# Optimization experiments

Measured on AMD Instinct MI355X. Metric: run time of the kernel, lower is better.

## Reference

```python
import jax, jax.numpy as jnp
import numpy as np

DIM = 64
HID = DIM // 8  # 8, hidden width of pos_fc / attn_fc
B, N, V = 1024, 64, 8
NUM_IDS = 10


def setup_inputs() -> dict:
    key = jax.random.key(0)
    ks = jax.random.split(key, 24)
    stdv = 1.0 / np.sqrt(DIM * DIM)
    inp = {
        "q": jax.random.normal(ks[0], (B, N, DIM), jnp.float32),
        "k": jax.random.normal(ks[1], (B, N, V, DIM), jnp.float32),
        "pos": jax.random.normal(ks[2], (B, N, V, 4), jnp.float32),
        "strength": jax.random.normal(ks[3], (512,), jnp.float32),
        # learned params
        "q_tbl": jax.random.uniform(ks[4], (NUM_IDS, DIM * DIM), jnp.float32, -stdv, stdv),
        "k_tbl": jax.random.uniform(ks[5], (NUM_IDS, DIM * DIM), jnp.float32, -stdv, stdv),
        "v_tbl": jax.random.uniform(ks[6], (NUM_IDS, DIM * DIM), jnp.float32, -stdv, stdv),
        "pos_w1": jax.random.normal(ks[7], (4, HID), jnp.float32) * 0.5,
        "pos_b1": jax.random.normal(ks[8], (HID,), jnp.float32) * 0.1,
        "pos_w2": jax.random.normal(ks[9], (HID, DIM), jnp.float32) * 0.2,
        "pos_b2": jax.random.normal(ks[10], (DIM,), jnp.float32) * 0.1,
        "attn_w1": jax.random.normal(ks[11], (DIM, HID), jnp.float32) * 0.1,
        "attn_b1": jax.random.normal(ks[12], (HID,), jnp.float32) * 0.1,
        "attn_w2": jax.random.normal(ks[13], (HID, DIM), jnp.float32) * 0.2,
        "attn_b2": jax.random.normal(ks[14], (DIM,), jnp.float32) * 0.1,
        "out_w": jax.random.normal(ks[15], (DIM, DIM), jnp.float32) * 0.1,
        "out_b": jax.random.normal(ks[16], (DIM,), jnp.float32) * 0.1,
        "str_w": jax.random.normal(ks[17], (512, DIM), jnp.float32) * 0.04,
        "str_b": jax.random.normal(ks[18], (DIM,), jnp.float32) * 0.1,
        # int args
        "mask": jax.random.randint(ks[19], (B, N, V, 1), 0, 2, jnp.int32),
        "embed_id1": 3,
    }
    return inp


def reference(q, k, pos, strength, q_tbl, k_tbl, v_tbl,
              pos_w1, pos_b1, pos_w2, pos_b2,
              attn_w1, attn_b1, attn_w2, attn_b2,
              out_w, out_b, str_w, str_b, mask, embed_id1):
    s = strength @ str_w + str_b                       # [DIM]
    Wq = q_tbl[embed_id1].reshape(DIM, DIM)
    Wk = k_tbl[embed_id1].reshape(DIM, DIM)
    Wv = v_tbl[embed_id1].reshape(DIM, DIM)
    # F.linear(x, W) = x @ W.T ; note v is computed from k (as in source)
    qh = q @ Wq.T + s                                  # [B,N,DIM]
    kh = k @ Wk.T + s                                  # [B,N,V,DIM]
    vh = k @ Wv.T + s                                  # [B,N,V,DIM]
    p = jax.nn.relu(pos @ pos_w1 + pos_b1) @ pos_w2 + pos_b2   # [B,N,V,DIM]
    attn = kh - qh[:, :, None, :] + p                  # [B,N,V,DIM]
    attn = jax.nn.relu(attn @ attn_w1 + attn_b1) @ attn_w2 + attn_b2
    attn = jnp.where(mask == 0, jnp.float32(-1e9), attn)
    attn = jax.nn.softmax(attn, axis=-2)               # softmax over views V
    x = ((vh + p) * attn).sum(axis=2)                  # [B,N,DIM]
    x = x @ out_w + out_b
    return x
```

## Files before the change

kernel.cpp:

```cpp
#include <hip/hip_runtime.h>

#define TBL 4096

#define WS_S    0
#define WS_AT   64
#define WS_BQT  (64 + 512)
#define WS_CT   (64 + 1024)
#define WS_C0   (64 + 1024 + 64)

typedef __attribute__((ext_vector_type(8))) short bf16x8;
typedef __attribute__((ext_vector_type(4))) float f32x4;

__device__ inline short f2bf(float f) {
    union { float f; unsigned u; } v; v.f = f;
    unsigned r = v.u + 0x7fffu + ((v.u >> 16) & 1u);
    return (short)(r >> 16);
}

__device__ inline bf16x8 pack8(const float* x) {
    bf16x8 r;
    #pragma unroll
    for (int i = 0; i < 8; ++i) r[i] = f2bf(x[i]);
    return r;
}

__device__ inline bf16x8 loadpack(const float* p) {
    float4 a = *(const float4*)p;
    float4 b = *(const float4*)(p + 4);
    float t[8] = {a.x, a.y, a.z, a.w, b.x, b.y, b.z, b.w};
    return pack8(t);
}

__device__ inline bf16x8 loadpackneg(const float* p) {
    float4 a = *(const float4*)p;
    float4 b = *(const float4*)(p + 4);
    float t[8] = {-a.x, -a.y, -a.z, -a.w, -b.x, -b.y, -b.z, -b.w};
    return pack8(t);
}

__global__ __launch_bounds__(256) void precompute_kernel(
    const float* __restrict__ strength, const float* __restrict__ str_w,
    const float* __restrict__ str_b,
    const float* __restrict__ q_tbl, const float* __restrict__ k_tbl,
    const float* __restrict__ attn_w1, const float* __restrict__ attn_b1,
    const float* __restrict__ pos_w2, const float* __restrict__ pos_b2,
    const int* __restrict__ embed_id, float* __restrict__ ws)
{
    __shared__ float red[4][64];
    const int t = threadIdx.x;
    const int blk = blockIdx.x;
    const int id = embed_id[0];
    if (blk == 0) {
        const int d = t & 63, part = t >> 6;
        float acc = 0.f;
        for (int i = part * 128; i < part * 128 + 128; ++i)
            acc += strength[i] * str_w[i * 64 + d];
        red[part][d] = acc;
        __syncthreads();
        if (t < 64)
            ws[WS_S + t] = red[0][t] + red[1][t] + red[2][t] + red[3][t] + str_b[t];
    } else if (blk <= 2) {
        const int h = (blk - 1) * 4 + (t >> 6);
        const int j = t & 63;
        const float* W = k_tbl + (size_t)id * TBL;
        float acc = 0.f;
        for (int d = 0; d < 64; ++d) acc += W[d * 64 + j] * attn_w1[d * 8 + h];
        ws[WS_AT + h * 64 + j] = acc;
    } else if (blk <= 4) {
        const int h = (blk - 3) * 4 + (t >> 6);
        const int j = t & 63;
        const float* W = q_tbl + (size_t)id * TBL;
        float acc = 0.f;
        for (int d = 0; d < 64; ++d) acc += W[d * 64 + j] * attn_w1[d * 8 + h];
        ws[WS_BQT + h * 64 + j] = acc;
    } else {
        if (t < 64) {
            const int h = t >> 3, g = t & 7;
            float acc = 0.f;
            for (int d = 0; d < 64; ++d) acc += pos_w2[g * 64 + d] * attn_w1[d * 8 + h];
            ws[WS_CT + t] = acc;
        } else if (t < 72) {
            const int h = t - 64;
            float acc = attn_b1[h];
            for (int d = 0; d < 64; ++d) acc += pos_b2[d] * attn_w1[d * 8 + h];
            ws[WS_C0 + h] = acc;
        }
    }
}

__global__ __launch_bounds__(256, 3) void attn2d_main(
    const float* __restrict__ q, const float* __restrict__ k,
    const float* __restrict__ pos, const float* __restrict__ v_tbl,
    const float* __restrict__ pos_w1, const float* __restrict__ pos_b1,
    const float* __restrict__ pos_w2, const float* __restrict__ pos_b2,
    const float* __restrict__ attn_w2, const float* __restrict__ attn_b2,
    const float* __restrict__ out_w, const float* __restrict__ out_b,
    const int* __restrict__ mask, const int* __restrict__ embed_id,
    const float* __restrict__ ws, float* __restrict__ out)
{
    __shared__ float rhid_lds[4][16 * 12];
    __shared__ float x_lds[4][8 * 68];

    const int tid  = threadIdx.x;
    const int lane = tid & 63;
    const int wiv  = __builtin_amdgcn_readfirstlane(tid >> 6);
    const int q4   = lane >> 4;
    const int col  = lane & 15;

    float* rh_w = rhid_lds[wiv];
    float* x_w  = x_lds[wiv];

    const int wid = blockIdx.x * 4 + wiv;
    const int id  = embed_id[0];

    bf16x8 Bv[4][2];
    #pragma unroll
    for (int t = 0; t < 4; ++t)
        #pragma unroll
        for (int c = 0; c < 2; ++c)
            Bv[t][c] = loadpack(v_tbl + (size_t)id * TBL +
                                (t * 16 + col) * 64 + c * 32 + q4 * 8);
    bf16x8 Bh[4];
    {
        bf16x8 z{};
        #pragma unroll
        for (int c = 0; c < 2; ++c)
            Bh[c] = (col < 8) ? loadpack(ws + WS_AT + col * 64 + c * 32 + q4 * 8) : z;
        #pragma unroll
        for (int c = 0; c < 2; ++c)
            Bh[2 + c] = (col < 8) ? loadpackneg(ws + WS_BQT + col * 64 + c * 32 + q4 * 8) : z;
    }
    bf16x8 Bct{};
    if (q4 == 0 && col < 8) Bct = loadpack(ws + WS_CT + col * 8);
    bf16x8 Bw2[4], Bpw2[4];
    {
        bf16x8 z{};
        #pragma unroll
        for (int t = 0; t < 4; ++t) {
            if (q4 == 0) {
                float t0[8], t1[8];
                #pragma unroll
                for (int j = 0; j < 8; ++j) {
                    t0[j] = attn_w2[j * 64 + t * 16 + col];
                    t1[j] = pos_w2[j * 64 + t * 16 + col];
                }
                Bw2[t] = pack8(t0); Bpw2[t] = pack8(t1);
            } else { Bw2[t] = z; Bpw2[t] = z; }
        }
    }

    float b2a4[4], sb4[4], ob4[4];
    #pragma unroll
    for (int t = 0; t < 4; ++t) {
        b2a4[t] = attn_b2[t * 16 + col];
        sb4[t]  = ws[WS_S + t * 16 + col] + pos_b2[t * 16 + col];
        ob4[t]  = out_b[t * 16 + col];
    }
    const float c0r = (col < 8) ? ws[WS_C0 + col] : 0.f;

    for (int it = 0; it < 4; ++it) {
        const int pair = wid * 4 + it;
        const int bn0  = pair * 2;

        bf16x8 Ak[2], Aq[2];
        #pragma unroll
        for (int c = 0; c < 2; ++c)
            Ak[c] = loadpack(k + ((size_t)pair * 16 + col) * 64 + c * 32 + q4 * 8);
        #pragma unroll
        for (int c = 0; c < 2; ++c)
            Aq[c] = loadpack(q + (size_t)(bn0 + (col >> 3)) * 64 + c * 32 + q4 * 8);

        const int4 mk = *(const int4*)(mask + (size_t)pair * 16 + q4 * 4);

        bf16x8 Ahp{};
        if (lane < 16) {
            float4 pp = *(const float4*)(pos + ((size_t)pair * 16 + lane) * 4);
            float hv[8];
            #pragma unroll
            for (int g = 0; g < 8; ++g)
                hv[g] = fmaxf(pos_b1[g] + pp.x * pos_w1[g] + pp.y * pos_w1[8 + g] +
                              pp.z * pos_w1[16 + g] + pp.w * pos_w1[24 + g], 0.f);
            Ahp = pack8(hv);
        }

        f32x4 acch = {0.f, 0.f, 0.f, 0.f};
        acch = __builtin_amdgcn_mfma_f32_16x16x32_bf16(Ak[0], Bh[0], acch, 0, 0, 0);
        acch = __builtin_amdgcn_mfma_f32_16x16x32_bf16(Ak[1], Bh[1], acch, 0, 0, 0);
        acch = __builtin_amdgcn_mfma_f32_16x16x32_bf16(Aq[0], Bh[2], acch, 0, 0, 0);
        acch = __builtin_amdgcn_mfma_f32_16x16x32_bf16(Aq[1], Bh[3], acch, 0, 0, 0);
        acch = __builtin_amdgcn_mfma_f32_16x16x32_bf16(Ahp,   Bct,   acch, 0, 0, 0);
        if (col < 8) {
            #pragma unroll
            for (int r = 0; r < 4; ++r)
                rh_w[(q4 * 4 + r) * 12 + col] = fmaxf(acch[r] + c0r, 0.f);
        }

        bf16x8 Arh{};
        if (lane < 16) Arh = loadpack(&rh_w[lane * 12]);

        #pragma unroll
        for (int t = 0; t < 4; ++t) {
            f32x4 av = {0.f, 0.f, 0.f, 0.f};
            av = __builtin_amdgcn_mfma_f32_16x16x32_bf16(Ak[0], Bv[t][0], av, 0, 0, 0);
            av = __builtin_amdgcn_mfma_f32_16x16x32_bf16(Ak[1], Bv[t][1], av, 0, 0, 0);
            av = __builtin_amdgcn_mfma_f32_16x16x32_bf16(Ahp,   Bpw2[t],  av, 0, 0, 0);
            f32x4 al = {0.f, 0.f, 0.f, 0.f};
            al = __builtin_amdgcn_mfma_f32_16x16x32_bf16(Arh, Bw2[t], al, 0, 0, 0);

            float att[4];
            att[0] = mk.x ? (al[0] + b2a4[t]) : -1e9f;
            att[1] = mk.y ? (al[1] + b2a4[t]) : -1e9f;
            att[2] = mk.z ? (al[2] + b2a4[t]) : -1e9f;
            att[3] = mk.w ? (al[3] + b2a4[t]) : -1e9f;

            float mp = fmaxf(fmaxf(att[0], att[1]), fmaxf(att[2], att[3]));
            float mm = fmaxf(mp, __shfl_xor(mp, 16));
            float e0 = __expf(att[0] - mm), e1 = __expf(att[1] - mm);
            float e2 = __expf(att[2] - mm), e3 = __expf(att[3] - mm);
            float sp = e0 + e1 + e2 + e3;
            float ss = sp + __shfl_xor(sp, 16);
            float xp = e0 * (av[0] + sb4[t]) + e1 * (av[1] + sb4[t])
                     + e2 * (av[2] + sb4[t]) + e3 * (av[3] + sb4[t]);
            float x = (xp + __shfl_xor(xp, 16)) * __builtin_amdgcn_rcpf(ss);
            if ((q4 & 1) == 0)
                x_w[(it * 2 + (q4 >> 1)) * 68 + t * 16 + col] = x;
        }
    }

    bf16x8 Ax[2]{};
    if (col < 8) {
        #pragma unroll
        for (int c = 0; c < 2; ++c)
            Ax[c] = loadpack(&x_w[col * 68 + c * 32 + q4 * 8]);
    }
    #pragma unroll
    for (int t = 0; t < 4; ++t) {
        bf16x8 Bo0, Bo1;
        {
            float t0[8], t1[8];
            #pragma unroll
            for (int jj = 0; jj < 8; ++jj) {
                t0[jj] = out_w[(q4 * 8 + jj) * 64 + t * 16 + col];
                t1[jj] = out_w[(32 + q4 * 8 + jj) * 64 + t * 16 + col];
            }
            Bo0 = pack8(t0); Bo1 = pack8(t1);
        }
        f32x4 a = {0.f, 0.f, 0.f, 0.f};
        a = __builtin_amdgcn_mfma_f32_16x16x32_bf16(Ax[0], Bo0, a, 0, 0, 0);
        a = __builtin_amdgcn_mfma_f32_16x16x32_bf16(Ax[1], Bo1, a, 0, 0, 0);
        #pragma unroll
        for (int r = 0; r < 4; ++r) {
            const int row = q4 * 4 + r;
            if (row < 8)
                out[((size_t)wid * 8 + row) * 64 + t * 16 + col] = a[r] + ob4[t];
        }
    }
}

extern "C" void kernel_launch(void* const* d_in, const int* in_sizes, int n_in,
                              void* d_out, int out_size, void* d_ws, size_t ws_size,
                              hipStream_t stream) {
    const float* q        = (const float*)d_in[0];
    const float* k        = (const float*)d_in[1];
    const float* pos      = (const float*)d_in[2];
    const float* strength = (const float*)d_in[3];
    const float* q_tbl    = (const float*)d_in[4];
    const float* k_tbl    = (const float*)d_in[5];
    const float* v_tbl    = (const float*)d_in[6];
    const float* pos_w1   = (const float*)d_in[7];
    const float* pos_b1   = (const float*)d_in[8];
    const float* pos_w2   = (const float*)d_in[9];
    const float* pos_b2   = (const float*)d_in[10];
    const float* attn_w1  = (const float*)d_in[11];
    const float* attn_b1  = (const float*)d_in[12];
    const float* attn_w2  = (const float*)d_in[13];
    const float* attn_b2  = (const float*)d_in[14];
    const float* out_w    = (const float*)d_in[15];
    const float* out_b    = (const float*)d_in[16];
    const float* str_w    = (const float*)d_in[17];
    const float* str_b    = (const float*)d_in[18];
    const int*   mask     = (const int*)d_in[19];
    const int*   embed    = (const int*)d_in[20];
    float* ws  = (float*)d_ws;
    float* out = (float*)d_out;

    hipLaunchKernelGGL(precompute_kernel, dim3(6), dim3(256), 0, stream,
                       strength, str_w, str_b, q_tbl, k_tbl, attn_w1, attn_b1,
                       pos_w2, pos_b2, embed, ws);
    hipLaunchKernelGGL(attn2d_main, dim3(2048), dim3(256), 0, stream,
                       q, k, pos, v_tbl, pos_w1, pos_b1, pos_w2, pos_b2,
                       attn_w2, attn_b2, out_w, out_b, mask, embed, ws, out);
}
```

Before: 291.0 us.

## Prepack bf16 weights, double-buffer k loads, process 8 pairs per wave

Adds a pack kernel that converts the weight matrices (v table, out_w, attn/pos weights) to bf16 in MFMA-ready layout once, so each wave loads them directly instead of gathering and converting floats. The main kernel now handles 16 rows per wave over 8 iterations with a grid of half the size, and prefetches the next iteration's k, pos and mask into registers. The q projection is computed once per wave, the pos MLP first layer moves onto MFMA, and k is truncated to bf16 via byte permutes instead of rounding. It costs an extra kernel launch and more registers, and the truncation slightly changes numerics.

Result: no change. 292.9 us (+0.6%).

```diff
diff --git a/kernel.cpp b/kernel.cpp
--- a/kernel.cpp
+++ b/kernel.cpp
@@ -4,9 +4,19 @@
 
 #define WS_S    0
 #define WS_AT   64
-#define WS_BQT  (64 + 512)
-#define WS_CT   (64 + 1024)
-#define WS_C0   (64 + 1024 + 64)
+#define WS_BQT  576
+#define WS_CT   1088
+#define WS_C0   1152
+#define WS_F32_END 1536
+#define PB_AT   0
+#define PB_BQN  512
+#define PB_CT   1024
+#define PB_W2T  1088
+#define PB_PW2T 1600
+#define PB_PW1  2112
+#define PB_VT   2176
+#define PB_OWT  6272
+#define PB_END  10368
 
 typedef __attribute__((ext_vector_type(8))) short bf16x8;
 typedef __attribute__((ext_vector_type(4))) float f32x4;
@@ -31,11 +41,13 @@
     return pack8(t);
 }
 
-__device__ inline bf16x8 loadpackneg(const float* p) {
-    float4 a = *(const float4*)p;
-    float4 b = *(const float4*)(p + 4);
-    float t[8] = {-a.x, -a.y, -a.z, -a.w, -b.x, -b.y, -b.z, -b.w};
-    return pack8(t);
+__device__ inline bf16x8 pack8t(float4 a, float4 b) {
+    union { unsigned u[4]; bf16x8 v; } r;
+    r.u[0] = __builtin_amdgcn_perm(__float_as_uint(a.y), __float_as_uint(a.x), 0x07060302u);
+    r.u[1] = __builtin_amdgcn_perm(__float_as_uint(a.w), __float_as_uint(a.z), 0x07060302u);
+    r.u[2] = __builtin_amdgcn_perm(__float_as_uint(b.y), __float_as_uint(b.x), 0x07060302u);
+    r.u[3] = __builtin_amdgcn_perm(__float_as_uint(b.w), __float_as_uint(b.z), 0x07060302u);
+    return r.v;
 }
 
 __global__ __launch_bounds__(256) void precompute_kernel(
@@ -88,18 +100,51 @@
     }
 }
 
+__global__ __launch_bounds__(256) void pack_kernel(
+    const float* __restrict__ v_tbl,
+    const float* __restrict__ pos_w1, const float* __restrict__ pos_w2,
+    const float* __restrict__ attn_w2, const float* __restrict__ out_w,
+    const int* __restrict__ embed_id, float* __restrict__ ws)
+{
+    short* pk = (short*)(ws + WS_F32_END);
+    const int i = blockIdx.x * 256 + threadIdx.x;
+    if (i >= PB_END) return;
+    const int id = embed_id[0];
+    if (i < 512) {
+        pk[i] = f2bf(ws[WS_AT + i]);
+    } else if (i < 1024) {
+        pk[i] = f2bf(-ws[WS_BQT + (i - 512)]);
+    } else if (i < 1088) {
+        pk[i] = f2bf(ws[WS_CT + (i - 1024)]);
+    } else if (i < 1600) {
+        const int idx = i - 1088, d = idx >> 3, h = idx & 7;
+        pk[i] = f2bf(attn_w2[h * 64 + d]);
+    } else if (i < 2112) {
+        const int idx = i - 1600, d = idx >> 3, h = idx & 7;
+        pk[i] = f2bf(pos_w2[h * 64 + d]);
+    } else if (i < 2176) {
+        const int idx = i - 2112, h = idx >> 3, j = idx & 7;
+        pk[i] = (j < 4) ? f2bf(pos_w1[j * 8 + h]) : (short)0;
+    } else if (i < 6272) {
+        pk[i] = f2bf(v_tbl[(size_t)id * TBL + (i - 2176)]);
+    } else {
+        const int idx = i - 6272, e = idx >> 6, d = idx & 63;
+        pk[i] = f2bf(out_w[d * 64 + e]);
+    }
+}
+
 __global__ __launch_bounds__(256, 3) void attn2d_main(
     const float* __restrict__ q, const float* __restrict__ k,
-    const float* __restrict__ pos, const float* __restrict__ v_tbl,
-    const float* __restrict__ pos_w1, const float* __restrict__ pos_b1,
-    const float* __restrict__ pos_w2, const float* __restrict__ pos_b2,
-    const float* __restrict__ attn_w2, const float* __restrict__ attn_b2,
-    const float* __restrict__ out_w, const float* __restrict__ out_b,
-    const int* __restrict__ mask, const int* __restrict__ embed_id,
+    const float* __restrict__ pos,
+    const float* __restrict__ pos_b1, const float* __restrict__ pos_b2,
+    const float* __restrict__ attn_b2, const float* __restrict__ out_b,
+    const int* __restrict__ mask,
     const float* __restrict__ ws, float* __restrict__ out)
 {
-    __shared__ float rhid_lds[4][16 * 12];
-    __shared__ float x_lds[4][8 * 68];
+    __shared__ __align__(16) short hp_bf[4][16 * 8];
+    __shared__ __align__(16) short rh_bf[4][16 * 8];
+    __shared__ __align__(16) float qB_lds[4][16 * 8];
+    __shared__ __align__(16) short x_bf[4][16 * 72];
 
     const int tid  = threadIdx.x;
     const int lane = tid & 63;
@@ -107,46 +152,32 @@
     const int q4   = lane >> 4;
     const int col  = lane & 15;
 
-    float* rh_w = rhid_lds[wiv];
-    float* x_w  = x_lds[wiv];
+    short* hp_w = hp_bf[wiv];
+    short* rh_w = rh_bf[wiv];
+    float* qB_w = qB_lds[wiv];
+    short* x_w  = x_bf[wiv];
 
     const int wid = blockIdx.x * 4 + wiv;
-    const int id  = embed_id[0];
+    const short* pk = (const short*)(ws + WS_F32_END);
+    const bf16x8 z{};
 
     bf16x8 Bv[4][2];
     #pragma unroll
     for (int t = 0; t < 4; ++t)
         #pragma unroll
         for (int c = 0; c < 2; ++c)
-            Bv[t][c] = loadpack(v_tbl + (size_t)id * TBL +
-                                (t * 16 + col) * 64 + c * 32 + q4 * 8);
-    bf16x8 Bh[4];
-    {
-        bf16x8 z{};
-        #pragma unroll
-        for (int c = 0; c < 2; ++c)
-            Bh[c] = (col < 8) ? loadpack(ws + WS_AT + col * 64 + c * 32 + q4 * 8) : z;
-        #pragma unroll
-        for (int c = 0; c < 2; ++c)
-            Bh[2 + c] = (col < 8) ? loadpackneg(ws + WS_BQT + col * 64 + c * 32 + q4 * 8) : z;
-    }
-    bf16x8 Bct{};
-    if (q4 == 0 && col < 8) Bct = loadpack(ws + WS_CT + col * 8);
+            Bv[t][c] = *(const bf16x8*)&pk[PB_VT + (t * 16 + col) * 64 + c * 32 + q4 * 8];
+    bf16x8 Bh[2];
+    #pragma unroll
+    for (int c = 0; c < 2; ++c)
+        Bh[c] = (col < 8) ? *(const bf16x8*)&pk[PB_AT + col * 64 + c * 32 + q4 * 8] : z;
+    const bf16x8 Bct  = (q4 == 0 && col < 8) ? *(const bf16x8*)&pk[PB_CT + col * 8] : z;
+    const bf16x8 Bpw1 = (q4 == 0 && col < 8) ? *(const bf16x8*)&pk[PB_PW1 + col * 8] : z;
     bf16x8 Bw2[4], Bpw2[4];
-    {
-        bf16x8 z{};
-        #pragma unroll
-        for (int t = 0; t < 4; ++t) {
-            if (q4 == 0) {
-                float t0[8], t1[8];
-                #pragma unroll
-                for (int j = 0; j < 8; ++j) {
-                    t0[j] = attn_w2[j * 64 + t * 16 + col];
-                    t1[j] = pos_w2[j * 64 + t * 16 + col];
-                }
-                Bw2[t] = pack8(t0); Bpw2[t] = pack8(t1);
-            } else { Bw2[t] = z; Bpw2[t] = z; }
-        }
+    #pragma unroll
+    for (int t = 0; t < 4; ++t) {
+        Bw2[t]  = (q4 == 0) ? *(const bf16x8*)&pk[PB_W2T  + (t * 16 + col) * 8] : z;
+        Bpw2[t] = (q4 == 0) ? *(const bf16x8*)&pk[PB_PW2T + (t * 16 + col) * 8] : z;
     }
 
     float b2a4[4], sb4[4], ob4[4];
@@ -157,61 +188,88 @@
         ob4[t]  = out_b[t * 16 + col];
     }
     const float c0r = (col < 8) ? ws[WS_C0 + col] : 0.f;
-
-    for (int it = 0; it < 4; ++it) {
-        const int pair = wid * 4 + it;
-        const int bn0  = pair * 2;
-
-        bf16x8 Ak[2], Aq[2];
-        #pragma unroll
-        for (int c = 0; c < 2; ++c)
-            Ak[c] = loadpack(k + ((size_t)pair * 16 + col) * 64 + c * 32 + q4 * 8);
-        #pragma unroll
-        for (int c = 0; c < 2; ++c)
-            Aq[c] = loadpack(q + (size_t)(bn0 + (col >> 3)) * 64 + c * 32 + q4 * 8);
-
-        const int4 mk = *(const int4*)(mask + (size_t)pair * 16 + q4 * 4);
-
-        bf16x8 Ahp{};
-        if (lane < 16) {
-            float4 pp = *(const float4*)(pos + ((size_t)pair * 16 + lane) * 4);
-            float hv[8];
+    const float b1c = (col < 8) ? pos_b1[col] : 0.f;
+
+    {
+        bf16x8 Bq0 = (col < 8) ? *(const bf16x8*)&pk[PB_BQN + col * 64 + q4 * 8] : z;
+        bf16x8 Bq1 = (col < 8) ? *(const bf16x8*)&pk[PB_BQN + col * 64 + 32 + q4 * 8] : z;
+        bf16x8 Aq0 = loadpack(q + (size_t)(wid * 16 + col) * 64 + q4 * 8);
+        bf16x8 Aq1 = loadpack(q + (size_t)(wid * 16 + col) * 64 + 32 + q4 * 8);
+        f32x4 aq = {0.f, 0.f, 0.f, 0.f};
+        aq = __builtin_amdgcn_mfma_f32_16x16x32_bf16(Aq0, Bq0, aq, 0, 0, 0);
+        aq = __builtin_amdgcn_mfma_f32_16x16x32_bf16(Aq1, Bq1, aq, 0, 0, 0);
+        if (col < 8) {
             #pragma unroll
-            for (int g = 0; g < 8; ++g)
-                hv[g] = fmaxf(pos_b1[g] + pp.x * pos_w1[g] + pp.y * pos_w1[8 + g] +
-                              pp.z * pos_w1[16 + g] + pp.w * pos_w1[24 + g], 0.f);
-            Ahp = pack8(hv);
-        }
-
-        f32x4 acch = {0.f, 0.f, 0.f, 0.f};
-        acch = __builtin_amdgcn_mfma_f32_16x16x32_bf16(Ak[0], Bh[0], acch, 0, 0, 0);
-        acch = __builtin_amdgcn_mfma_f32_16x16x32_bf16(Ak[1], Bh[1], acch, 0, 0, 0);
-        acch = __builtin_amdgcn_mfma_f32_16x16x32_bf16(Aq[0], Bh[2], acch, 0, 0, 0);
-        acch = __builtin_amdgcn_mfma_f32_16x16x32_bf16(Aq[1], Bh[3], acch, 0, 0, 0);
-        acch = __builtin_amdgcn_mfma_f32_16x16x32_bf16(Ahp,   Bct,   acch, 0, 0, 0);
+            for (int r = 0; r < 4; ++r) qB_w[(q4 * 4 + r) * 8 + col] = aq[r];
+        }
+    }
+
+    float4 kr[2][2][2]; float4 pr[2]; int4 mr[2];
+    auto issue = [&](int b, int it2) {
+        const size_t pair = (size_t)wid * 8 + it2;
+        const float* kb = k + (pair * 16 + col) * 64 + q4 * 8;
+        kr[b][0][0] = *(const float4*)kb;
+        kr[b][0][1] = *(const float4*)(kb + 4);
+        kr[b][1][0] = *(const float4*)(kb + 32);
+        kr[b][1][1] = *(const float4*)(kb + 36);
+        pr[b] = (q4 == 0) ? *(const float4*)(pos + (pair * 16 + col) * 4)
+                          : make_float4(0.f, 0.f, 0.f, 0.f);
+        mr[b] = *(const int4*)(mask + pair * 16 + q4 * 4);
+    };
+    issue(0, 0);
+
+    #pragma unroll 2
+    for (int it = 0; it < 8; ++it) {
+        const int b = it & 1;
+        if (it < 7) issue(b ^ 1, it + 1);
+        const int rowbase = it * 2 + (q4 >> 1);
+
+        bf16x8 Apos = z;
+        if (q4 == 0) {
+            float t4[8] = {pr[b].x, pr[b].y, pr[b].z, pr[b].w, 0.f, 0.f, 0.f, 0.f};
+            Apos = pack8(t4);
+        }
+        f32x4 hpc = {0.f, 0.f, 0.f, 0.f};
+        hpc = __builtin_amdgcn_mfma_f32_16x16x32_bf16(Apos, Bpw1, hpc, 0, 0, 0);
         if (col < 8) {
             #pragma unroll
             for (int r = 0; r < 4; ++r)
-                rh_w[(q4 * 4 + r) * 12 + col] = fmaxf(acch[r] + c0r, 0.f);
-        }
-
-        bf16x8 Arh{};
-        if (lane < 16) Arh = loadpack(&rh_w[lane * 12]);
+                hp_w[(q4 * 4 + r) * 8 + col] = f2bf(fmaxf(hpc[r] + b1c, 0.f));
+        }
+
+        bf16x8 Ak0 = pack8t(kr[b][0][0], kr[b][0][1]);
+        bf16x8 Ak1 = pack8t(kr[b][1][0], kr[b][1][1]);
+
+        bf16x8 Ahp = z;
+        if (lane < 16) Ahp = *(const bf16x8*)&hp_w[lane * 8];
+
+        const float qbc = (col < 8) ? qB_w[rowbase * 8 + col] : 0.f;
+        f32x4 acch = {0.f, 0.f, 0.f, 0.f};
+        acch = __builtin_amdgcn_mfma_f32_16x16x32_bf16(Ak0, Bh[0], acch, 0, 0, 0);
+        acch = __builtin_amdgcn_mfma_f32_16x16x32_bf16(Ak1, Bh[1], acch, 0, 0, 0);
+        acch = __builtin_amdgcn_mfma_f32_16x16x32_bf16(Ahp, Bct,  acch, 0, 0, 0);
+        if (col < 8) {
+            #pragma unroll
+            for (int r = 0; r < 4; ++r)
+                rh_w[(q4 * 4 + r) * 8 + col] = f2bf(fmaxf(acch[r] + qbc + c0r, 0.f));
+        }
+        bf16x8 Arh = z;
+        if (lane < 16) Arh = *(const bf16x8*)&rh_w[lane * 8];
 
         #pragma unroll
         for (int t = 0; t < 4; ++t) {
             f32x4 av = {0.f, 0.f, 0.f, 0.f};
-            av = __builtin_amdgcn_mfma_f32_16x16x32_bf16(Ak[0], Bv[t][0], av, 0, 0, 0);
-            av = __builtin_amdgcn_mfma_f32_16x16x32_bf16(Ak[1], Bv[t][1], av, 0, 0, 0);
-            av = __builtin_amdgcn_mfma_f32_16x16x32_bf16(Ahp,   Bpw2[t],  av, 0, 0, 0);
+            av = __builtin_amdgcn_mfma_f32_16x16x32_bf16(Ak0, Bv[t][0], av, 0, 0, 0);
+            av = __builtin_amdgcn_mfma_f32_16x16x32_bf16(Ak1, Bv[t][1], av, 0, 0, 0);
+            av = __builtin_amdgcn_mfma_f32_16x16x32_bf16(Ahp, Bpw2[t],  av, 0, 0, 0);
             f32x4 al = {0.f, 0.f, 0.f, 0.f};
             al = __builtin_amdgcn_mfma_f32_16x16x32_bf16(Arh, Bw2[t], al, 0, 0, 0);
 
             float att[4];
-            att[0] = mk.x ? (al[0] + b2a4[t]) : -1e9f;
-            att[1] = mk.y ? (al[1] + b2a4[t]) : -1e9f;
-            att[2] = mk.z ? (al[2] + b2a4[t]) : -1e9f;
-            att[3] = mk.w ? (al[3] + b2a4[t]) : -1e9f;
+            att[0] = mr[b].x ? (al[0] + b2a4[t]) : -1e9f;
+            att[1] = mr[b].y ? (al[1] + b2a4[t]) : -1e9f;
+            att[2] = mr[b].z ? (al[2] + b2a4[t]) : -1e9f;
+            att[3] = mr[b].w ? (al[3] + b2a4[t]) : -1e9f;
 
             float mp = fmaxf(fmaxf(att[0], att[1]), fmaxf(att[2], att[3]));
             float mm = fmaxf(mp, __shfl_xor(mp, 16));
@@ -223,37 +281,24 @@
                      + e2 * (av[2] + sb4[t]) + e3 * (av[3] + sb4[t]);
             float x = (xp + __shfl_xor(xp, 16)) * __builtin_amdgcn_rcpf(ss);
             if ((q4 & 1) == 0)
-                x_w[(it * 2 + (q4 >> 1)) * 68 + t * 16 + col] = x;
-        }
-    }
-
-    bf16x8 Ax[2]{};
-    if (col < 8) {
-        #pragma unroll
-        for (int c = 0; c < 2; ++c)
-            Ax[c] = loadpack(&x_w[col * 68 + c * 32 + q4 * 8]);
-    }
+                x_w[rowbase * 72 + t * 16 + col] = f2bf(x);
+        }
+    }
+
+    bf16x8 Ax[2];
+    #pragma unroll
+    for (int c = 0; c < 2; ++c)
+        Ax[c] = *(const bf16x8*)&x_w[col * 72 + c * 32 + q4 * 8];
     #pragma unroll
     for (int t = 0; t < 4; ++t) {
-        bf16x8 Bo0, Bo1;
-        {
-            float t0[8], t1[8];
-            #pragma unroll
-            for (int jj = 0; jj < 8; ++jj) {
-                t0[jj] = out_w[(q4 * 8 + jj) * 64 + t * 16 + col];
-                t1[jj] = out_w[(32 + q4 * 8 + jj) * 64 + t * 16 + col];
-            }
-            Bo0 = pack8(t0); Bo1 = pack8(t1);
-        }
+        bf16x8 Bo0 = *(const bf16x8*)&pk[PB_OWT + (t * 16 + col) * 64 + q4 * 8];
+        bf16x8 Bo1 = *(const bf16x8*)&pk[PB_OWT + (t * 16 + col) * 64 + 32 + q4 * 8];
         f32x4 a = {0.f, 0.f, 0.f, 0.f};
         a = __builtin_amdgcn_mfma_f32_16x16x32_bf16(Ax[0], Bo0, a, 0, 0, 0);
         a = __builtin_amdgcn_mfma_f32_16x16x32_bf16(Ax[1], Bo1, a, 0, 0, 0);
         #pragma unroll
-        for (int r = 0; r < 4; ++r) {
-            const int row = q4 * 4 + r;
-            if (row < 8)
-                out[((size_t)wid * 8 + row) * 64 + t * 16 + col] = a[r] + ob4[t];
-        }
+        for (int r = 0; r < 4; ++r)
+            out[((size_t)wid * 16 + q4 * 4 + r) * 64 + t * 16 + col] = a[r] + ob4[t];
     }
 }
 
@@ -287,7 +332,8 @@
     hipLaunchKernelGGL(precompute_kernel, dim3(6), dim3(256), 0, stream,
                        strength, str_w, str_b, q_tbl, k_tbl, attn_w1, attn_b1,
                        pos_w2, pos_b2, embed, ws);
-    hipLaunchKernelGGL(attn2d_main, dim3(2048), dim3(256), 0, stream,
-                       q, k, pos, v_tbl, pos_w1, pos_b1, pos_w2, pos_b2,
-                       attn_w2, attn_b2, out_w, out_b, mask, embed, ws, out);
-}
+    hipLaunchKernelGGL(pack_kernel, dim3((PB_END + 255) / 256), dim3(256), 0, stream,
+                       v_tbl, pos_w1, pos_w2, attn_w2, out_w, embed, ws);
+    hipLaunchKernelGGL(attn2d_main, dim3(1024), dim3(256), 0, stream,
+                       q, k, pos, pos_b1, pos_b2, attn_b2, out_b, mask, ws, out);
+}
```
